# Kernel optimization log

Hardware: AMD Instinct MI355X
Metric: run time of the kernel (lower is better)

Reference implementation:

```python
import jax, jax.numpy as jnp
import numpy as np

D_MODEL = 1024
N_HEADS = 16
N_KV_HEADS = 4
HEAD_DIM = D_MODEL // N_HEADS
NUM_REP = N_HEADS // N_KV_HEADS
B, T = 2, 2048


def setup_inputs() -> dict:
    key = jax.random.key(0)
    ks = jax.random.split(key, 9)
    s = 0.02
    x = jax.random.normal(ks[0], (B, T, D_MODEL), dtype=jnp.float32)
    # causal mask: True = masked (matches torch masked_fill semantics)
    mask = jnp.triu(jnp.ones((T, T), dtype=bool), k=1)[None, None]
    kv_dim = N_KV_HEADS * HEAD_DIM
    return {
        "x": x,
        "mask": mask,
        "Wq": jax.random.normal(ks[1], (D_MODEL, D_MODEL), jnp.float32) * s,
        "bq": jnp.zeros((D_MODEL,), jnp.float32),
        "Wk": jax.random.normal(ks[2], (D_MODEL, kv_dim), jnp.float32) * s,
        "bk": jnp.zeros((kv_dim,), jnp.float32),
        "Wv": jax.random.normal(ks[3], (D_MODEL, kv_dim), jnp.float32) * s,
        "bv": jnp.zeros((kv_dim,), jnp.float32),
        "Wo": jax.random.normal(ks[4], (D_MODEL, D_MODEL), jnp.float32) * s,
        "bo": jnp.zeros((D_MODEL,), jnp.float32),
    }


def reference(x, mask, Wq, bq, Wk, bk, Wv, bv, Wo, bo):
    Bx, Tx, C = x.shape
    # projections
    q = (x @ Wq + bq).reshape(Bx, Tx, N_HEADS, HEAD_DIM).transpose(0, 2, 1, 3)  # (B,H,T,D)
    k = (x @ Wk + bk).reshape(Bx, Tx, N_KV_HEADS, HEAD_DIM)
    v = (x @ Wv + bv).reshape(Bx, Tx, N_KV_HEADS, HEAD_DIM)
    # repeat_kv: expand+reshape == repeat along head axis
    k = jnp.repeat(k, NUM_REP, axis=2).transpose(0, 2, 1, 3)  # (B,H,T,D)
    v = jnp.repeat(v, NUM_REP, axis=2).transpose(0, 2, 1, 3)
    scale = 1.0 / jnp.sqrt(jnp.asarray(HEAD_DIM, x.dtype))
    attn = jnp.einsum('bhtd,bhsd->bhts', q, k) * scale  # (B,H,T,T)
    attn = jnp.where(mask, -jnp.inf, attn)
    attn = jax.nn.softmax(attn, axis=-1)
    out = jnp.einsum('bhts,bhsd->bhtd', attn, v)
    out = out.transpose(0, 2, 1, 3).reshape(Bx, Tx, C)
    return out @ Wo + bo
```

## Files before the change

### kernel.cpp

```cpp
#include <hip/hip_runtime.h>
#include <hip/hip_bf16.h>
#include <cmath>
#include <stdint.h>


typedef __attribute__((ext_vector_type(4))) float f32x4;
typedef __attribute__((ext_vector_type(16))) float f32x16;
typedef __attribute__((ext_vector_type(8))) short s16x8;
typedef __attribute__((ext_vector_type(8))) unsigned short u16x8;

#define MFMA32(a, b, c) __builtin_amdgcn_mfma_f32_32x32x16_bf16(a, b, c, 0, 0, 0)

__device__ __forceinline__ unsigned short f2bf(float f) {
    unsigned int u = __float_as_uint(f);
    u += 0x7FFFu + ((u >> 16) & 1u);
    return (unsigned short)(u >> 16);
}

__device__ __forceinline__ unsigned int pktr(float lo, float hi) {
    return __builtin_amdgcn_perm(__float_as_uint(hi), __float_as_uint(lo), 0x07060302u);
}

__device__ __forceinline__ void async16(void* lds, const void* g) {
    __builtin_amdgcn_global_load_lds(
        (const __attribute__((address_space(1))) unsigned int*)g,
        (__attribute__((address_space(3))) unsigned int*)lds, 16, 0, 0);
}

__global__ __launch_bounds__(256) void prep(
        const float* __restrict__ x,
        const float* __restrict__ Wq, const float* __restrict__ Wk,
        const float* __restrict__ Wv, const float* __restrict__ Wo,
        const float* __restrict__ bq, const float* __restrict__ bk,
        const float* __restrict__ bv,
        unsigned short* __restrict__ xb, unsigned short* __restrict__ Wqkv,
        unsigned short* __restrict__ Wot, float* __restrict__ biasq, float qscale) {
    __shared__ unsigned short sx[128 * 72];
    __shared__ float tile[32][33];
    const int bid = blockIdx.x, tid = threadIdx.x;
    if (bid < 512) {
        const int mt = bid >> 4, kt = bid & 15;
#pragma unroll
        for (int i = 0; i < 8; ++i) {
            const int flat = (i * 256 + tid) * 4;
            const int row = flat >> 6, col = flat & 63;
            f32x4 ld = *reinterpret_cast<const f32x4*>(
                &x[(size_t)(mt * 128 + row) * 1024 + kt * 64 + col]);
            unsigned short* d = &sx[row * 72 + col];
            d[0] = f2bf(ld.x); d[1] = f2bf(ld.y); d[2] = f2bf(ld.z); d[3] = f2bf(ld.w);
        }
        __syncthreads();
#pragma unroll
        for (int j = 0; j < 4; ++j) {
            const int idx = j * 256 + tid;
            const int kb = idx >> 7, m = idx & 127;
            u16x8 v = *reinterpret_cast<const u16x8*>(&sx[m * 72 + kb * 8]);
            *reinterpret_cast<u16x8*>(
                &xb[(size_t)(((mt * 16 + kt) * 8 + kb) * 128 + m) * 8]) = v;
        }
    } else if (bid < 3072) {
        int id = bid - 512;
        const float* W; unsigned short* out; int N, nbase; float scale = 1.0f;
        if (id < 1024)      { W = Wq; out = Wqkv; N = 1024; nbase = 0;    scale = qscale; }
        else if (id < 1280) { W = Wk; out = Wqkv; N = 256;  nbase = 1024; id -= 1024; }
        else if (id < 1536) { W = Wv; out = Wqkv; N = 256;  nbase = 1280; id -= 1280; }
        else                { W = Wo; out = Wot;  N = 1024; nbase = 0;    id -= 1536; }
        const int nb = N >> 5;
        const int n0 = (id % nb) * 32, k0 = (id / nb) * 32;
        const int tx = tid & 31, ty = tid >> 5;
#pragma unroll
        for (int r = 0; r < 4; ++r)
            tile[ty + r * 8][tx] = W[(size_t)(k0 + ty + r * 8) * N + n0 + tx];
        __syncthreads();
        const int k = k0 + tx;
#pragma unroll
        for (int r = 0; r < 4; ++r) {
            const int n = nbase + n0 + ty + r * 8;
            size_t addr = (size_t)((n >> 6) * 16 + (k >> 6)) * 4096
                        + (size_t)((((k >> 3) & 7) * 64 + (n & 63)) * 8 + (k & 7));
            out[addr] = f2bf(tile[tx][ty + r * 8] * scale);
        }
    } else {
        const int i = (bid - 3072) * 256 + tid;
        if (i < 1024) biasq[i] = bq[i] * qscale;
        else if (i < 1280) biasq[i] = bk[i - 1024];
        else biasq[i] = bv[i - 1280];
    }
}

template <int EPI>
__global__ __launch_bounds__(256) void gemm_mn(
        const unsigned short* __restrict__ A, const unsigned short* __restrict__ Bt,
        const float* __restrict__ bias,
        unsigned short* __restrict__ oQ, unsigned short* __restrict__ oK,
        unsigned short* __restrict__ oV, float* __restrict__ oF) {
    __shared__ alignas(16) unsigned short smem[24576];
    const int tid = threadIdx.x;
    const int lane = tid & 63, w = tid >> 6;
    const int l31 = lane & 31, grp = lane >> 5;
    const int m0 = blockIdx.y * 128, n0 = blockIdx.x * 64;
    const int wm = w * 32;

    const unsigned short* Abase = A + (size_t)blockIdx.y * (16 * 8192) + (size_t)tid * 8;
    const unsigned short* Bbase = Bt + (size_t)blockIdx.x * (16 * 4096) + (size_t)tid * 8;

    f32x16 acc0 = {}, acc1 = {};

#pragma unroll
    for (int i = 0; i < 4; ++i)
        async16(&smem[(size_t)(i * 256 + (tid & 192)) * 8], Abase + (size_t)i * 2048);
#pragma unroll
    for (int i = 0; i < 2; ++i)
        async16(&smem[16384 + (size_t)(i * 256 + (tid & 192)) * 8], Bbase + (size_t)i * 2048);

    for (int kt = 0; kt < 16; ++kt) {
        const int cur = kt & 1;
        unsigned short* cA = smem + cur * 8192;
        unsigned short* cB = smem + 16384 + cur * 4096;
        __syncthreads();
        if (kt < 15) {
            unsigned short* nA = smem + (cur ^ 1) * 8192;
            unsigned short* nB = smem + 16384 + (cur ^ 1) * 4096;
            const unsigned short* ab = Abase + (size_t)(kt + 1) * 8192;
            const unsigned short* bb = Bbase + (size_t)(kt + 1) * 4096;
#pragma unroll
            for (int i = 0; i < 4; ++i)
                async16(&nA[(size_t)(i * 256 + (tid & 192)) * 8], ab + (size_t)i * 2048);
#pragma unroll
            for (int i = 0; i < 2; ++i)
                async16(&nB[(size_t)(i * 256 + (tid & 192)) * 8], bb + (size_t)i * 2048);
        }
#pragma unroll
        for (int kc = 0; kc < 4; ++kc) {
            const int kb = kc * 2 + grp;
            s16x8 a  = *reinterpret_cast<const s16x8*>(&cA[(size_t)(kb * 128 + wm + l31) * 8]);
            s16x8 b0 = *reinterpret_cast<const s16x8*>(&cB[(size_t)(kb * 64 + l31) * 8]);
            s16x8 b1 = *reinterpret_cast<const s16x8*>(&cB[(size_t)(kb * 64 + 32 + l31) * 8]);
            acc0 = MFMA32(a, b0, acc0);
            acc1 = MFMA32(a, b1, acc1);
        }
    }
    const float bv0 = bias[n0 + l31], bv1 = bias[n0 + 32 + l31];
    if (EPI == 0 && n0 >= 1280) {
        __syncthreads();
#pragma unroll
        for (int r = 0; r < 16; ++r) {
            const int m = wm + (r & 3) + 8 * (r >> 2) + 4 * grp;
            smem[(size_t)l31 * 136 + m] = f2bf(acc0[r] + bv0);
            smem[(size_t)(l31 + 32) * 136 + m] = f2bf(acc1[r] + bv1);
        }
        __syncthreads();
#pragma unroll
        for (int i = 0; i < 4; ++i) {
            const int id = i * 256 + tid;
            const int n = id >> 4, mc = id & 15;
            u16x8 v = *reinterpret_cast<const u16x8*>(&smem[(size_t)n * 136 + mc * 8]);
            *reinterpret_cast<u16x8*>(&oV[(size_t)(n0 - 1280 + n) * 4096 + m0 + mc * 8]) = v;
        }
        return;
    }
#pragma unroll
    for (int r = 0; r < 16; ++r) {
        const int row = m0 + wm + (r & 3) + 8 * (r >> 2) + 4 * grp;
        const float v0 = acc0[r] + bv0, v1 = acc1[r] + bv1;
        if (EPI == 0) {
            if (n0 < 1024) {
                oQ[(size_t)row * 1024 + n0 + l31] = f2bf(v0);
                oQ[(size_t)row * 1024 + n0 + 32 + l31] = f2bf(v1);
            } else {
                oK[(size_t)row * 256 + (n0 - 1024) + l31] = f2bf(v0);
                oK[(size_t)row * 256 + (n0 - 1024) + 32 + l31] = f2bf(v1);
            }
        } else {
            oF[(size_t)row * 1024 + n0 + l31] = v0;
            oF[(size_t)row * 1024 + n0 + 32 + l31] = v1;
        }
    }
}

__global__ __launch_bounds__(128) void flash_attn(
        const unsigned short* __restrict__ Qb, const unsigned short* __restrict__ Kb,
        const unsigned short* __restrict__ Vt, unsigned short* __restrict__ Ot) {
    __shared__ float sO[64][33];
    __shared__ float sL[64];
    const int tid = threadIdx.x;
    const int lane = tid & 63, w = tid >> 6;
    const int ln = lane & 31, grp = lane >> 5;
    const int id = blockIdx.x;
    const int kvh = id & 3;
    const int b = (id >> 2) & 1;
    const int h = kvh * 4 + ((id >> 3) & 3);
    const int strip = 63 - (id >> 5);
    const int t0w = strip * 32;
    const int qrow_g = t0w + ln;
    const int nch = (strip >> 1) + 1;

    const unsigned short* Qrow = Qb + (size_t)(b * 2048 + qrow_g) * 1024 + h * 64;
    s16x8 qf[4];
#pragma unroll
    for (int kk = 0; kk < 4; ++kk)
        qf[kk] = *reinterpret_cast<const s16x8*>(Qrow + kk * 16 + grp * 8);

    const unsigned short* Kp = Kb + (size_t)(b * 2048) * 256 + kvh * 64;
    const unsigned short* Vp = Vt + (size_t)(kvh * 64) * 4096 + (size_t)b * 2048;
    const unsigned short* kr0 = Kp + (size_t)ln * 256 + grp * 8;
    const unsigned short* kr1 = Kp + (size_t)(32 + ln) * 256 + grp * 8;
    const unsigned short* vr0 = Vp + (size_t)ln * 4096 + grp * 8;
    const unsigned short* vr1 = Vp + (size_t)(32 + ln) * 4096 + grp * 8;

    f32x16 o0 = {}, o1 = {};
    float ltot = 0.f;

    for (int c = w; c < nch; c += 2) {
        const int s0 = c * 64;
        s16x8 kf0[4], kf1[4], vf0[4], vf1[4];
#pragma unroll
        for (int kk = 0; kk < 4; ++kk) {
            kf0[kk] = *reinterpret_cast<const s16x8*>(kr0 + (size_t)s0 * 256 + kk * 16);
            kf1[kk] = *reinterpret_cast<const s16x8*>(kr1 + (size_t)s0 * 256 + kk * 16);
            vf0[kk] = *reinterpret_cast<const s16x8*>(vr0 + s0 + kk * 16);
            vf1[kk] = *reinterpret_cast<const s16x8*>(vr1 + s0 + kk * 16);
        }
        f32x16 st0 = {}, st1 = {};
#pragma unroll
        for (int kk = 0; kk < 4; ++kk) {
            st0 = MFMA32(kf0[kk], qf[kk], st0);
            st1 = MFMA32(kf1[kk], qf[kk], st1);
        }
        if (s0 + 63 > t0w) {
#pragma unroll
            for (int r = 0; r < 16; ++r) {
                const int keyo = s0 + (r & 3) + 8 * (r >> 2) + 4 * grp;
                if (keyo > qrow_g)      st0[r] = -INFINITY;
                if (keyo + 32 > qrow_g) st1[r] = -INFINITY;
            }
        }
        f32x16 p0, p1;
#pragma unroll
        for (int r = 0; r < 16; ++r) {
            p0[r] = __builtin_amdgcn_exp2f(st0[r]);
            p1[r] = __builtin_amdgcn_exp2f(st1[r]);
        }
        float a0 = 0.f, a1 = 0.f, a2 = 0.f, a3 = 0.f;
#pragma unroll
        for (int r = 0; r < 16; r += 2) {
            a0 += p0[r]; a1 += p0[r + 1];
            a2 += p1[r]; a3 += p1[r + 1];
        }
        ltot += (a0 + a1) + (a2 + a3);
#pragma unroll
        for (int kkp = 0; kkp < 4; ++kkp) {
            const f32x16& pm = (kkp < 2) ? p0 : p1;
            const int A4 = 8 * (kkp & 1);
            unsigned int pA0 = pktr(pm[A4 + 0], pm[A4 + 1]);
            unsigned int pA1 = pktr(pm[A4 + 2], pm[A4 + 3]);
            unsigned int pB0 = pktr(pm[A4 + 4], pm[A4 + 5]);
            unsigned int pB1 = pktr(pm[A4 + 6], pm[A4 + 7]);
            unsigned int x0 = (unsigned int)__shfl_xor((int)(grp ? pA0 : pB0), 32, 64);
            unsigned int x1 = (unsigned int)__shfl_xor((int)(grp ? pA1 : pB1), 32, 64);
            union { unsigned int u[4]; s16x8 v; } pf;
            pf.u[0] = grp ? x0 : pA0;
            pf.u[1] = grp ? x1 : pA1;
            pf.u[2] = grp ? pB0 : x0;
            pf.u[3] = grp ? pB1 : x1;
            o0 = MFMA32(pf.v, vf0[kkp], o0);
            o1 = MFMA32(pf.v, vf1[kkp], o1);
        }
    }

    if (w == 1) {
#pragma unroll
        for (int r = 0; r < 16; ++r) {
            sO[lane][r] = o0[r];
            sO[lane][16 + r] = o1[r];
        }
        sL[lane] = ltot;
    }
    __syncthreads();
    if (w == 1) return;
#pragma unroll
    for (int r = 0; r < 16; ++r) {
        o0[r] += sO[lane][r];
        o1[r] += sO[lane][16 + r];
    }
    ltot += sL[lane];

    const float lfull = ltot + __shfl_xor(ltot, 32, 64);
    const float rl = 1.0f / lfull;
    unsigned short* Otb = Ot + (size_t)((b * 16 + (strip >> 2)) * 16 + h) * 8192
                             + (size_t)(ln >> 3) * 1024 + (ln & 7);
#pragma unroll
    for (int r = 0; r < 16; ++r) {
        const int row = (r & 3) + 8 * (r >> 2) + 4 * grp;
        const float rr = __shfl(rl, row, 64);
        const size_t off = (size_t)((strip & 3) * 32 + row) * 8;
        Otb[off]        = f2bf(o0[r] * rr);
        Otb[off + 4096] = f2bf(o1[r] * rr);
    }
}

extern "C" void kernel_launch(void* const* d_in, const int* in_sizes, int n_in,
                              void* d_out, int out_size, void* d_ws, size_t ws_size,
                              hipStream_t stream) {
    const float* x  = (const float*)d_in[0];
    const float* Wq = (const float*)d_in[2];
    const float* bq = (const float*)d_in[3];
    const float* Wk = (const float*)d_in[4];
    const float* bk = (const float*)d_in[5];
    const float* Wv = (const float*)d_in[6];
    const float* bv = (const float*)d_in[7];
    const float* Wo = (const float*)d_in[8];
    const float* bo = (const float*)d_in[9];
    float* out = (float*)d_out;

    char* ws = (char*)d_ws;
    unsigned short* xb    = (unsigned short*)(ws);
    unsigned short* Wqkv  = (unsigned short*)(ws + (8u  << 20));
    unsigned short* Wot   = (unsigned short*)(ws + (12u << 20));
    float*          biasq = (float*)         (ws + (15u << 20));
    unsigned short* Qb    = (unsigned short*)(ws + (16u << 20));
    unsigned short* Kb    = (unsigned short*)(ws + (24u << 20));
    unsigned short* Vtp   = (unsigned short*)(ws + (26u << 20));
    unsigned short* Otl   = (unsigned short*)(ws + (28u << 20));

    const float qscale = 0.125f * 1.4426950408889634f;

    prep<<<3078, 256, 0, stream>>>(x, Wq, Wk, Wv, Wo, bq, bk, bv,
                                   xb, Wqkv, Wot, biasq, qscale);
    gemm_mn<0><<<dim3(24, 32), 256, 0, stream>>>(xb, Wqkv, biasq, Qb, Kb, Vtp, nullptr);
    flash_attn<<<2048, 128, 0, stream>>>(Qb, Kb, Vtp, Otl);
    gemm_mn<1><<<dim3(16, 32), 256, 0, stream>>>(Otl, Wot, bo, nullptr, nullptr, nullptr, out);
}
```

Before: 194.4 us.

## Store K and V in MFMA-fragment tiled layout so attention loads are contiguous

The QKV GEMM epilogue now writes K and V through shared memory into a per-(batch, kv-head, 64-key chunk) tiled layout. In that layout each lane's 16-byte fragment for the attention MFMAs sits contiguously, so consecutive lanes hit consecutive 16-byte addresses. The flash attention kernel's K/V loads change from strided row accesses (stride 256 or 4096 elements) to fully coalesced chunk loads. This adds an LDS staging round-trip and extra barriers in the K epilogue of the projection GEMM.

```diff
diff --git a/kernel.cpp b/kernel.cpp
--- a/kernel.cpp
+++ b/kernel.cpp
@@ -143,6 +143,7 @@
     const float bv0 = bias[n0 + l31], bv1 = bias[n0 + 32 + l31];
     if (EPI == 0 && n0 >= 1280) {
         __syncthreads();
+        const int kvh = (n0 - 1280) >> 6;
 #pragma unroll
         for (int r = 0; r < 16; ++r) {
             const int m = wm + (r & 3) + 8 * (r >> 2) + 4 * grp;
@@ -150,12 +151,37 @@
             smem[(size_t)(l31 + 32) * 136 + m] = f2bf(acc1[r] + bv1);
         }
         __syncthreads();
+        const int b = m0 >> 11, c0 = (m0 & 2047) >> 6;
+        unsigned short* vb = oV + (size_t)((b * 4 + kvh) * 32 + c0) * 4096;
 #pragma unroll
         for (int i = 0; i < 4; ++i) {
             const int id = i * 256 + tid;
-            const int n = id >> 4, mc = id & 15;
-            u16x8 v = *reinterpret_cast<const u16x8*>(&smem[(size_t)n * 136 + mc * 8]);
-            *reinterpret_cast<u16x8*>(&oV[(size_t)(n0 - 1280 + n) * 4096 + m0 + mc * 8]) = v;
+            const int d = id >> 4, mc = id & 15;
+            u16x8 v = *reinterpret_cast<const u16x8*>(&smem[(size_t)d * 136 + mc * 8]);
+            *reinterpret_cast<u16x8*>(&vb[(size_t)(mc >> 3) * 4096
+                + ((size_t)(mc & 7) * 64 + d) * 8]) = v;
+        }
+        return;
+    }
+    if (EPI == 0 && n0 >= 1024) {
+        __syncthreads();
+        const int kvh = (n0 - 1024) >> 6;
+#pragma unroll
+        for (int r = 0; r < 16; ++r) {
+            const int m = wm + (r & 3) + 8 * (r >> 2) + 4 * grp;
+            smem[(size_t)m * 72 + l31] = f2bf(acc0[r] + bv0);
+            smem[(size_t)m * 72 + 32 + l31] = f2bf(acc1[r] + bv1);
+        }
+        __syncthreads();
+        const int b = m0 >> 11, c0 = (m0 & 2047) >> 6;
+        unsigned short* kb_o = oK + (size_t)((b * 4 + kvh) * 32 + c0) * 4096;
+#pragma unroll
+        for (int i = 0; i < 4; ++i) {
+            const int id = i * 256 + tid;
+            const int si = id >> 3, dc = id & 7;
+            u16x8 v = *reinterpret_cast<const u16x8*>(&smem[(size_t)si * 72 + dc * 8]);
+            *reinterpret_cast<u16x8*>(&kb_o[(size_t)(si >> 6) * 4096
+                + ((size_t)dc * 64 + (si & 63)) * 8]) = v;
         }
         return;
     }
@@ -164,13 +190,8 @@
         const int row = m0 + wm + (r & 3) + 8 * (r >> 2) + 4 * grp;
         const float v0 = acc0[r] + bv0, v1 = acc1[r] + bv1;
         if (EPI == 0) {
-            if (n0 < 1024) {
-                oQ[(size_t)row * 1024 + n0 + l31] = f2bf(v0);
-                oQ[(size_t)row * 1024 + n0 + 32 + l31] = f2bf(v1);
-            } else {
-                oK[(size_t)row * 256 + (n0 - 1024) + l31] = f2bf(v0);
-                oK[(size_t)row * 256 + (n0 - 1024) + 32 + l31] = f2bf(v1);
-            }
+            oQ[(size_t)row * 1024 + n0 + l31] = f2bf(v0);
+            oQ[(size_t)row * 1024 + n0 + 32 + l31] = f2bf(v1);
         } else {
             oF[(size_t)row * 1024 + n0 + l31] = v0;
             oF[(size_t)row * 1024 + n0 + 32 + l31] = v1;
@@ -179,8 +200,8 @@
 }
 
 __global__ __launch_bounds__(128) void flash_attn(
-        const unsigned short* __restrict__ Qb, const unsigned short* __restrict__ Kb,
-        const unsigned short* __restrict__ Vt, unsigned short* __restrict__ Ot) {
+        const unsigned short* __restrict__ Qb, const unsigned short* __restrict__ Ktl,
+        const unsigned short* __restrict__ Vtl, unsigned short* __restrict__ Ot) {
     __shared__ float sO[64][33];
     __shared__ float sL[64];
     const int tid = threadIdx.x;
@@ -201,25 +222,28 @@
     for (int kk = 0; kk < 4; ++kk)
         qf[kk] = *reinterpret_cast<const s16x8*>(Qrow + kk * 16 + grp * 8);
 
-    const unsigned short* Kp = Kb + (size_t)(b * 2048) * 256 + kvh * 64;
-    const unsigned short* Vp = Vt + (size_t)(kvh * 64) * 4096 + (size_t)b * 2048;
-    const unsigned short* kr0 = Kp + (size_t)ln * 256 + grp * 8;
-    const unsigned short* kr1 = Kp + (size_t)(32 + ln) * 256 + grp * 8;
-    const unsigned short* vr0 = Vp + (size_t)ln * 4096 + grp * 8;
-    const unsigned short* vr1 = Vp + (size_t)(32 + ln) * 4096 + grp * 8;
+    const unsigned short* Kc = Ktl + (size_t)((b * 4 + kvh) * 32) * 4096
+                                   + ((size_t)grp * 64 + ln) * 8;
+    const unsigned short* Vc = Vtl + (size_t)((b * 4 + kvh) * 32) * 4096
+                                   + ((size_t)grp * 64 + ln) * 8;
 
     f32x16 o0 = {}, o1 = {};
     float ltot = 0.f;
 
     for (int c = w; c < nch; c += 2) {
         const int s0 = c * 64;
+        const unsigned short* kc = Kc + (size_t)c * 4096;
+        const unsigned short* vc = Vc + (size_t)c * 4096;
         s16x8 kf0[4], kf1[4], vf0[4], vf1[4];
 #pragma unroll
         for (int kk = 0; kk < 4; ++kk) {
-            kf0[kk] = *reinterpret_cast<const s16x8*>(kr0 + (size_t)s0 * 256 + kk * 16);
-            kf1[kk] = *reinterpret_cast<const s16x8*>(kr1 + (size_t)s0 * 256 + kk * 16);
-            vf0[kk] = *reinterpret_cast<const s16x8*>(vr0 + s0 + kk * 16);
-            vf1[kk] = *reinterpret_cast<const s16x8*>(vr1 + s0 + kk * 16);
+            kf0[kk] = *reinterpret_cast<const s16x8*>(kc + kk * 1024);
+            kf1[kk] = *reinterpret_cast<const s16x8*>(kc + kk * 1024 + 256);
+        }
+#pragma unroll
+        for (int kk = 0; kk < 4; ++kk) {
+            vf0[kk] = *reinterpret_cast<const s16x8*>(vc + kk * 1024);
+            vf1[kk] = *reinterpret_cast<const s16x8*>(vc + kk * 1024 + 256);
         }
         f32x16 st0 = {}, st1 = {};
 #pragma unroll
@@ -319,15 +343,15 @@
     unsigned short* Wot   = (unsigned short*)(ws + (12u << 20));
     float*          biasq = (float*)         (ws + (15u << 20));
     unsigned short* Qb    = (unsigned short*)(ws + (16u << 20));
-    unsigned short* Kb    = (unsigned short*)(ws + (24u << 20));
-    unsigned short* Vtp   = (unsigned short*)(ws + (26u << 20));
+    unsigned short* Ktl   = (unsigned short*)(ws + (24u << 20));
+    unsigned short* Vtl   = (unsigned short*)(ws + (26u << 20));
     unsigned short* Otl   = (unsigned short*)(ws + (28u << 20));
 
     const float qscale = 0.125f * 1.4426950408889634f;
 
     prep<<<3078, 256, 0, stream>>>(x, Wq, Wk, Wv, Wo, bq, bk, bv,
                                    xb, Wqkv, Wot, biasq, qscale);
-    gemm_mn<0><<<dim3(24, 32), 256, 0, stream>>>(xb, Wqkv, biasq, Qb, Kb, Vtp, nullptr);
-    flash_attn<<<2048, 128, 0, stream>>>(Qb, Kb, Vtp, Otl);
+    gemm_mn<0><<<dim3(24, 32), 256, 0, stream>>>(xb, Wqkv, biasq, Qb, Ktl, Vtl, nullptr);
+    flash_attn<<<2048, 128, 0, stream>>>(Qb, Ktl, Vtl, Otl);
     gemm_mn<1><<<dim3(16, 32), 256, 0, stream>>>(Otl, Wot, bo, nullptr, nullptr, nullptr, out);
 }
```

Result: faster. 164.8 us (-15.2%).
